# Performance work log

Hardware: AMD Instinct MI355X
Metric: run time of the kernel (lower is better)

Reference implementation:

```python
import jax, jax.numpy as jnp
import numpy as np

B, NQ, NC, DC, DY = 4, 4096, 4096, 2, 8


def setup_inputs() -> dict:
    key = jax.random.key(0)
    k1, k2, k3 = jax.random.split(key, 3)
    x_query = jax.random.normal(k1, (B, NQ, DC), dtype=jnp.float32)
    x_context = jax.random.normal(k2, (B, NC, DC), dtype=jnp.float32)
    y_context = jax.random.normal(k3, (B, NC, DY), dtype=jnp.float32)
    log_length_scale = jnp.asarray(np.log(0.1), dtype=jnp.float32)
    return {
        "x_query": x_query,
        "x_context": x_context,
        "y_context": y_context,
        "log_length_scale": log_length_scale,
    }


def reference(x_query, x_context, y_context, log_length_scale):
    # Squared Euclidean distances: (B, NQ, NC).
    # cdist followed by .pow(2) == squared distance, so compute d2 directly.
    diff = x_query[:, :, None, :] - x_context[:, None, :, :]  # (B,NQ,NC,DC)
    d2 = jnp.sum(diff * diff, axis=-1)                         # (B,NQ,NC)
    length_scale = jnp.exp(log_length_scale)
    weights = jnp.exp(-d2 / (2.0 * length_scale ** 2))         # RBF kernel
    density = jnp.sum(weights, axis=-1, keepdims=True)         # (B,NQ,1)
    weights_norm = weights / (density + 1e-8)
    y_query = jnp.einsum('bqc,bcd->bqd', weights_norm, y_context)  # (B,NQ,DY)
    return jnp.concatenate([y_query, density], axis=-1)        # (B,NQ,DY+1)
```

## Files before the change

### kernel.cpp

```cpp
#include <hip/hip_runtime.h>


#define BB 4
#define NQ 4096
#define NC 4096
#define DY 8
#define NBQ (BB * NQ)

#if __has_builtin(__builtin_amdgcn_exp2f)
#define EXP2F(x) __builtin_amdgcn_exp2f(x)
#else
#define EXP2F(x) exp2f(x)
#endif

typedef short bf16x8 __attribute__((ext_vector_type(8)));
typedef float f32x4  __attribute__((ext_vector_type(4)));

#define GSPLIT 8
#define CCHUNK (NC / GSPLIT)
#define WCTX (CCHUNK / 4)
#define KSTEPS (WCTX / 32)
#define QPB 32
#define QB (NBQ / QPB)
#define JS ((size_t)GSPLIT * NBQ)
#define WS_FLOATS ((size_t)(DY + 1) * GSPLIT * NBQ)

__device__ __forceinline__ short f2bf(float v) {
    return (short)(__builtin_bit_cast(unsigned, v) >> 16);
}

__global__ __launch_bounds__(256, 4) void setconv_accum_mfma(
    const float* __restrict__ xq, const float* __restrict__ xc,
    const float* __restrict__ yc, const float* __restrict__ lls,
    float* __restrict__ ws)
{
    __shared__ float4 sctx[CCHUNK];
    __shared__ float  red[4][QPB][DY + 1];

    const int bid  = blockIdx.x;
    const int gs   = bid & (GSPLIT - 1);
    const int qb   = bid >> 3;
    const int b    = qb >> 7;
    const int tid  = threadIdx.x;
    const int lane = tid & 63;
    const int wv   = tid >> 6;
    const int n    = lane & 15;
    const int quad = lane >> 4;

    const float L    = lls[0];
    const float negk = -0.72134752044448f * EXP2F(L * -2.8853900817779268f);

    {
        const float2* xcp = ((const float2*)xc) + (size_t)b * NC + gs * CCHUNK;
        for (int i = tid; i < CCHUNK; i += 256) {
            const float2 cv = xcp[i];
            sctx[i] = make_float4(cv.x, cv.y,
                                  negk * fmaf(cv.x, cv.x, cv.y * cv.y), 0.f);
        }
    }

    float a0[2], a1[2], a2[2];
#pragma unroll
    for (int t = 0; t < 2; ++t) {
        const float2 qv = ((const float2*)xq)[(size_t)qb * QPB + t * 16 + n];
        a0[t] = negk * fmaf(qv.x, qv.x, qv.y * qv.y);
        a1[t] = -2.f * negk * qv.x;
        a2[t] = -2.f * negk * qv.y;
    }

    f32x4 acc0 = {0.f, 0.f, 0.f, 0.f};
    f32x4 acc1 = {0.f, 0.f, 0.f, 0.f};

    __syncthreads();

    const float* __restrict__ ycb = yc + (size_t)b * NC * DY;
    const int w0 = wv * WCTX;

#pragma unroll
    for (int s = 0; s < KSTEPS; ++s) {
        const int kb = w0 + s * 32 + quad * 8;

        float yv[8];
#pragma unroll
        for (int j = 0; j < 8; ++j) {
            const int c = gs * CCHUNK + kb + j;
            float v = 0.f;
            if (n < 8)       v = ycb[(size_t)c * DY + n];
            else if (n == 8) v = 1.0f;
            yv[j] = v;
        }

        bf16x8 af0, af1, bf;
#pragma unroll
        for (int j = 0; j < 8; ++j) {
            const float4 cv = sctx[kb + j];
            const float base = cv.z;
            float t0 = a0[0] + base;
            t0 = fmaf(a2[0], cv.y, t0);
            t0 = fmaf(a1[0], cv.x, t0);
            float t1 = a0[1] + base;
            t1 = fmaf(a2[1], cv.y, t1);
            t1 = fmaf(a1[1], cv.x, t1);
            af0[j] = f2bf(EXP2F(t0));
            af1[j] = f2bf(EXP2F(t1));
            bf[j]  = f2bf(yv[j]);
        }
        acc0 = __builtin_amdgcn_mfma_f32_16x16x32_bf16(af0, bf, acc0, 0, 0, 0);
        acc1 = __builtin_amdgcn_mfma_f32_16x16x32_bf16(af1, bf, acc1, 0, 0, 0);
    }

    if (n <= 8) {
#pragma unroll
        for (int r = 0; r < 4; ++r) {
            red[wv][quad * 4 + r][n]      = acc0[r];
            red[wv][16 + quad * 4 + r][n] = acc1[r];
        }
    }
    __syncthreads();

    for (int v = tid; v < QPB * (DY + 1); v += 256) {
        const int ql = v / (DY + 1);
        const int j  = v - ql * (DY + 1);
        const float s = red[0][ql][j] + red[1][ql][j] +
                        red[2][ql][j] + red[3][ql][j];
        ws[(size_t)j * JS + (size_t)gs * NBQ + (size_t)qb * QPB + ql] = s;
    }
}

__global__ __launch_bounds__(256) void setconv_reduce(
    const float* __restrict__ ws, float* __restrict__ out)
{
    __shared__ float part[4][64][DY + 1];
    const int tid  = threadIdx.x;
    const int qi   = tid & 63;
    const int sg   = tid >> 6;
    const int base = blockIdx.x * 64;
    const int bq   = base + qi;

#pragma unroll
    for (int j = 0; j < DY + 1; ++j) {
        float s = 0.f;
#pragma unroll
        for (int k = 0; k < GSPLIT / 4; ++k) {
            const int split = sg * (GSPLIT / 4) + k;
            s += ws[(size_t)j * JS + (size_t)split * NBQ + bq];
        }
        part[sg][qi][j] = s;
    }
    __syncthreads();

    for (int it = tid; it < 64 * (DY + 1); it += 256) {
        const int q2 = it / (DY + 1);
        const int j  = it - q2 * (DY + 1);
        const float den = part[0][q2][DY] + part[1][q2][DY] +
                          part[2][q2][DY] + part[3][q2][DY];
        float v;
        if (j == DY) {
            v = den;
        } else {
            const float s = part[0][q2][j] + part[1][q2][j] +
                            part[2][q2][j] + part[3][q2][j];
            v = s / (den + 1e-8f);
        }
        out[(size_t)base * (DY + 1) + it] = v;
    }
}

#define FSPLIT 8
#define FCCH (NC / FSPLIT)

__global__ __launch_bounds__(256) void setconv_zero(float4* __restrict__ out) {
    out[blockIdx.x * 256 + threadIdx.x] = make_float4(0.f, 0.f, 0.f, 0.f);
}

__global__ __launch_bounds__(256) void setconv_accum_atomic(
    const float* __restrict__ xq, const float* __restrict__ xc,
    const float* __restrict__ yc, const float* __restrict__ lls,
    float* __restrict__ out)
{
    const int bid   = blockIdx.x;
    const int split = bid & (FSPLIT - 1);
    const int qblk  = (bid / FSPLIT) & (NQ / 256 - 1);
    const int b     = bid / (FSPLIT * (NQ / 256));
    const int q     = qblk * 256 + threadIdx.x;

    const float L    = lls[0];
    const float negk = -0.72134752044448f * EXP2F(L * -2.8853900817779268f);

    const float2 qv = ((const float2*)xq)[b * NQ + q];
    const float qx0 = qv.x, qy0 = qv.y;

    float acc[DY], den = 0.f;
#pragma unroll
    for (int j = 0; j < DY; ++j) acc[j] = 0.f;

    const float2* __restrict__ xcp = ((const float2*)xc) + (size_t)b * NC;
    const float4* __restrict__ ycp = ((const float4*)yc) + (size_t)b * NC * 2;

    const int c0 = split * FCCH;
#pragma unroll 4
    for (int c = c0; c < c0 + FCCH; ++c) {
        const float2 cv = xcp[c];
        const float4 y0 = ycp[2 * c + 0];
        const float4 y1 = ycp[2 * c + 1];
        const float dx = qx0 - cv.x;
        const float dy = qy0 - cv.y;
        const float d2 = fmaf(dy, dy, dx * dx);
        const float w  = EXP2F(d2 * negk);
        den += w;
        acc[0] = fmaf(w, y0.x, acc[0]);
        acc[1] = fmaf(w, y0.y, acc[1]);
        acc[2] = fmaf(w, y0.z, acc[2]);
        acc[3] = fmaf(w, y0.w, acc[3]);
        acc[4] = fmaf(w, y1.x, acc[4]);
        acc[5] = fmaf(w, y1.y, acc[5]);
        acc[6] = fmaf(w, y1.z, acc[6]);
        acc[7] = fmaf(w, y1.w, acc[7]);
    }

    float* o = out + (size_t)(b * NQ + q) * (DY + 1);
#pragma unroll
    for (int j = 0; j < DY; ++j) atomicAdd(o + j, acc[j]);
    atomicAdd(o + DY, den);
}

__global__ __launch_bounds__(256) void setconv_norm(float* __restrict__ out) {
    const int q = blockIdx.x * 256 + threadIdx.x;
    float* o = out + (size_t)q * (DY + 1);
    const float inv = 1.0f / (o[DY] + 1e-8f);
#pragma unroll
    for (int j = 0; j < DY; ++j) o[j] *= inv;
}

extern "C" void kernel_launch(void* const* d_in, const int* in_sizes, int n_in,
                              void* d_out, int out_size, void* d_ws, size_t ws_size,
                              hipStream_t stream) {
    const float* xq  = (const float*)d_in[0];
    const float* xc  = (const float*)d_in[1];
    const float* yc  = (const float*)d_in[2];
    const float* lls = (const float*)d_in[3];
    float* out = (float*)d_out;

    if (ws_size >= WS_FLOATS * sizeof(float)) {
        float* ws = (float*)d_ws;
        setconv_accum_mfma<<<QB * GSPLIT, 256, 0, stream>>>(xq, xc, yc, lls, ws);
        setconv_reduce<<<NBQ / 64, 256, 0, stream>>>(ws, out);
    } else {
        setconv_zero<<<(NBQ * (DY + 1)) / 1024, 256, 0, stream>>>((float4*)out);
        setconv_accum_atomic<<<BB * (NQ / 256) * FSPLIT, 256, 0, stream>>>(xq, xc, yc, lls, out);
        setconv_norm<<<NBQ / 256, 256, 0, stream>>>(out);
    }
}
```

Before: 81.26 us.

## Give each wave its own queries and stage bf16 y fragments in LDS

After: 73.81 us. 9.2% less time.

```diff
diff --git a/kernel.cpp b/kernel.cpp
--- a/kernel.cpp
+++ b/kernel.cpp
@@ -16,35 +16,35 @@
 typedef short bf16x8 __attribute__((ext_vector_type(8)));
 typedef float f32x4  __attribute__((ext_vector_type(4)));
 
+__device__ __forceinline__ short f2bf(float v) {
+    return (short)(__builtin_bit_cast(unsigned, v) >> 16);
+}
+
 #define GSPLIT 8
 #define CCHUNK (NC / GSPLIT)
-#define WCTX (CCHUNK / 4)
-#define KSTEPS (WCTX / 32)
-#define QPB 32
+#define KSTEPS (CCHUNK / 32)
+#define QPB 128
 #define QB (NBQ / QPB)
 #define JS ((size_t)GSPLIT * NBQ)
 #define WS_FLOATS ((size_t)(DY + 1) * GSPLIT * NBQ)
-
-__device__ __forceinline__ short f2bf(float v) {
-    return (short)(__builtin_bit_cast(unsigned, v) >> 16);
-}
 
 __global__ __launch_bounds__(256, 4) void setconv_accum_mfma(
     const float* __restrict__ xq, const float* __restrict__ xc,
     const float* __restrict__ yc, const float* __restrict__ lls,
     float* __restrict__ ws)
 {
-    __shared__ float4 sctx[CCHUNK];
-    __shared__ float  red[4][QPB][DY + 1];
+    __shared__ float2 sxy[CCHUNK];
+    __shared__ float  shc[CCHUNK];
+    __shared__ unsigned short yfrag[CCHUNK / 8][16][8];
 
     const int bid  = blockIdx.x;
     const int gs   = bid & (GSPLIT - 1);
     const int qb   = bid >> 3;
-    const int b    = qb >> 7;
+    const int b    = qb >> 5;
     const int tid  = threadIdx.x;
     const int lane = tid & 63;
     const int wv   = tid >> 6;
-    const int n    = lane & 15;
+    const int m    = lane & 15;
     const int quad = lane >> 4;
 
     const float L    = lls[0];
@@ -52,17 +52,46 @@
 
     {
         const float2* xcp = ((const float2*)xc) + (size_t)b * NC + gs * CCHUNK;
-        for (int i = tid; i < CCHUNK; i += 256) {
-            const float2 cv = xcp[i];
-            sctx[i] = make_float4(cv.x, cv.y,
-                                  negk * fmaf(cv.x, cv.x, cv.y * cv.y), 0.f);
+#pragma unroll
+        for (int i = 0; i < 2; ++i) {
+            const int c = tid + 256 * i;
+            const float2 cv = xcp[c];
+            sxy[c] = cv;
+            shc[c] = negk * fmaf(cv.x, cv.x, cv.y * cv.y);
+        }
+    }
+    {
+        const float4* yp = (const float4*)(yc + ((size_t)b * NC + gs * CCHUNK) * DY);
+#pragma unroll
+        for (int i = 0; i < 2; ++i) {
+            const int c = tid + 256 * i;
+            const float4 A  = yp[2 * c + 0];
+            const float4 Bv = yp[2 * c + 1];
+            const int g = c >> 3, j = c & 7;
+            unsigned short* dst = &yfrag[g][0][j];
+            dst[0 * 8] = (unsigned short)f2bf(A.x);
+            dst[1 * 8] = (unsigned short)f2bf(A.y);
+            dst[2 * 8] = (unsigned short)f2bf(A.z);
+            dst[3 * 8] = (unsigned short)f2bf(A.w);
+            dst[4 * 8] = (unsigned short)f2bf(Bv.x);
+            dst[5 * 8] = (unsigned short)f2bf(Bv.y);
+            dst[6 * 8] = (unsigned short)f2bf(Bv.z);
+            dst[7 * 8] = (unsigned short)f2bf(Bv.w);
+        }
+        unsigned* yf32 = (unsigned*)yfrag;
+#pragma unroll
+        for (int i = 0; i < (CCHUNK / 8) * 32 / 256; ++i) {
+            const int v = tid + 256 * i;
+            const int g = v >> 5, r = v & 31;
+            yf32[g * 64 + 32 + r] = (r < 4) ? 0x3F803F80u : 0u;
         }
     }
 
     float a0[2], a1[2], a2[2];
 #pragma unroll
     for (int t = 0; t < 2; ++t) {
-        const float2 qv = ((const float2*)xq)[(size_t)qb * QPB + t * 16 + n];
+        const int q = qb * QPB + (wv * 2 + t) * 16 + m;
+        const float2 qv = ((const float2*)xq)[q];
         a0[t] = negk * fmaf(qv.x, qv.x, qv.y * qv.y);
         a1[t] = -2.f * negk * qv.x;
         a2[t] = -2.f * negk * qv.y;
@@ -73,57 +102,35 @@
 
     __syncthreads();
 
-    const float* __restrict__ ycb = yc + (size_t)b * NC * DY;
-    const int w0 = wv * WCTX;
-
-#pragma unroll
+#pragma unroll 4
     for (int s = 0; s < KSTEPS; ++s) {
-        const int kb = w0 + s * 32 + quad * 8;
-
-        float yv[8];
+        const bf16x8 bfrag = *(const bf16x8*)&yfrag[s * 4 + quad][m][0];
+        bf16x8 af0, af1;
 #pragma unroll
         for (int j = 0; j < 8; ++j) {
-            const int c = gs * CCHUNK + kb + j;
-            float v = 0.f;
-            if (n < 8)       v = ycb[(size_t)c * DY + n];
-            else if (n == 8) v = 1.0f;
-            yv[j] = v;
-        }
-
-        bf16x8 af0, af1, bf;
-#pragma unroll
-        for (int j = 0; j < 8; ++j) {
-            const float4 cv = sctx[kb + j];
-            const float base = cv.z;
-            float t0 = a0[0] + base;
+            const int c = s * 32 + quad * 8 + j;
+            const float2 cv = sxy[c];
+            const float hc = shc[c];
+            float t0 = a0[0] + hc;
             t0 = fmaf(a2[0], cv.y, t0);
             t0 = fmaf(a1[0], cv.x, t0);
-            float t1 = a0[1] + base;
+            float t1 = a0[1] + hc;
             t1 = fmaf(a2[1], cv.y, t1);
             t1 = fmaf(a1[1], cv.x, t1);
             af0[j] = f2bf(EXP2F(t0));
             af1[j] = f2bf(EXP2F(t1));
-            bf[j]  = f2bf(yv[j]);
-        }
-        acc0 = __builtin_amdgcn_mfma_f32_16x16x32_bf16(af0, bf, acc0, 0, 0, 0);
-        acc1 = __builtin_amdgcn_mfma_f32_16x16x32_bf16(af1, bf, acc1, 0, 0, 0);
-    }
-
-    if (n <= 8) {
+        }
+        acc0 = __builtin_amdgcn_mfma_f32_16x16x32_bf16(af0, bfrag, acc0, 0, 0, 0);
+        acc1 = __builtin_amdgcn_mfma_f32_16x16x32_bf16(af1, bfrag, acc1, 0, 0, 0);
+    }
+
+    if (m <= 8) {
+        const size_t base = (size_t)m * JS + (size_t)gs * NBQ + (size_t)qb * QPB;
 #pragma unroll
         for (int r = 0; r < 4; ++r) {
-            red[wv][quad * 4 + r][n]      = acc0[r];
-            red[wv][16 + quad * 4 + r][n] = acc1[r];
-        }
-    }
-    __syncthreads();
-
-    for (int v = tid; v < QPB * (DY + 1); v += 256) {
-        const int ql = v / (DY + 1);
-        const int j  = v - ql * (DY + 1);
-        const float s = red[0][ql][j] + red[1][ql][j] +
-                        red[2][ql][j] + red[3][ql][j];
-        ws[(size_t)j * JS + (size_t)gs * NBQ + (size_t)qb * QPB + ql] = s;
+            ws[base + (wv * 2 + 0) * 16 + quad * 4 + r] = acc0[r];
+            ws[base + (wv * 2 + 1) * 16 + quad * 4 + r] = acc1[r];
+        }
     }
 }
 
```
